# Kernel optimization log

Hardware: AMD Instinct MI355X
Metric: run time of the kernel (lower is better)

The kernel has to match this reference:

```python
import jax, jax.numpy as jnp
import numpy as np

B, C, H, W = 32, 3, 224, 224
P = 16                 # patch size
D = 768                # embed_size
NH = 12                # num heads
HD = D // NH           # head size
L = 12                 # depth
MLP = 4 * D
NC = 1000              # num classes
GH, GW = H // P, W // P
T = GH * GW            # tokens = 196
PATCH_DIM = P * P * C
EPS = 1e-5


def posemb_sincos_2d(h, w, dim, temperature=10000.0):
    yy, xx = jnp.meshgrid(jnp.arange(h, dtype=jnp.float32),
                          jnp.arange(w, dtype=jnp.float32), indexing='ij')
    omega = jnp.arange(dim // 4, dtype=jnp.float32) / (dim // 4 - 1)
    omega = 1.0 / (temperature ** omega)
    yv = yy.reshape(-1)[:, None] * omega[None, :]
    xv = xx.reshape(-1)[:, None] * omega[None, :]
    return jnp.concatenate([jnp.sin(xv), jnp.cos(xv), jnp.sin(yv), jnp.cos(yv)], axis=1)


def layernorm(x, g, b):
    mu = jnp.mean(x, axis=-1, keepdims=True)
    var = jnp.mean((x - mu) ** 2, axis=-1, keepdims=True)
    return (x - mu) * jax.lax.rsqrt(var + EPS) * g + b


def setup_inputs() -> dict:
    key = jax.random.key(0)
    ks = jax.random.split(key, 16)
    s = 0.02
    inp = {
        'x': jax.random.normal(ks[0], (B, C, H, W), jnp.float32),
        'embed_W': jax.random.normal(ks[1], (PATCH_DIM, D), jnp.float32) * s,
        'embed_b': jnp.zeros((D,), jnp.float32),
        'Wq': jax.random.normal(ks[2], (L, NH, D, HD), jnp.float32) * s,
        'Wk': jax.random.normal(ks[3], (L, NH, D, HD), jnp.float32) * s,
        'Wv': jax.random.normal(ks[4], (L, NH, D, HD), jnp.float32) * s,
        'Wo': jax.random.normal(ks[5], (L, D, D), jnp.float32) * s,
        'bo': jnp.zeros((L, D), jnp.float32),
        'ln1_g': jnp.ones((L, D), jnp.float32),
        'ln1_b': jnp.zeros((L, D), jnp.float32),
        'ln2_g': jnp.ones((L, D), jnp.float32),
        'ln2_b': jnp.zeros((L, D), jnp.float32),
        'W1': jax.random.normal(ks[6], (L, D, MLP), jnp.float32) * s,
        'b1': jnp.zeros((L, MLP), jnp.float32),
        'W2': jax.random.normal(ks[7], (L, MLP, D), jnp.float32) * s,
        'b2': jnp.zeros((L, D), jnp.float32),
        'head_W': jax.random.normal(ks[8], (D, NC), jnp.float32) * s,
    }
    return inp


def reference(x, embed_W, embed_b, Wq, Wk, Wv, Wo, bo,
              ln1_g, ln1_b, ln2_g, ln2_b, W1, b1, W2, b2, head_W):
    # patchify: b c (h p1) (w p2) -> b (h w) (p1 p2 c)
    p = x.reshape(B, C, GH, P, GW, P)
    p = p.transpose(0, 2, 4, 3, 5, 1).reshape(B, T, PATCH_DIM)
    h = p @ embed_W + embed_b + posemb_sincos_2d(GH, GW, D)[None]  # [B,T,D]

    scale = HD ** -0.5
    for l in range(L):
        xn = layernorm(h, ln1_g[l], ln1_b[l])
        q = jnp.einsum('btd,hde->bhte', xn, Wq[l])
        k = jnp.einsum('btd,hde->bhte', xn, Wk[l])
        v = jnp.einsum('btd,hde->bhte', xn, Wv[l])
        scores = jax.nn.softmax(jnp.einsum('bhte,bhse->bhts', q, k) * scale, axis=-1)
        att = jnp.einsum('bhts,bhse->bhte', scores, v)
        att = att.transpose(0, 2, 1, 3).reshape(B, T, D)  # concat heads
        h = h + att @ Wo[l] + bo[l]
        xn = layernorm(h, ln2_g[l], ln2_b[l])
        h = h + jax.nn.gelu(xn @ W1[l] + b1[l], approximate=False) @ W2[l] + b2[l]

    return h.mean(axis=1) @ head_W  # [B, NC]
```

## Files before the change

### kernel.cpp

```cpp
#include <hip/hip_runtime.h>
#include <cstdint>


typedef __bf16 bf16_t;
typedef __bf16 bf16x8 __attribute__((ext_vector_type(8)));
typedef __bf16 bf16x4 __attribute__((ext_vector_type(4)));
typedef float  f32x4  __attribute__((ext_vector_type(4)));

#define NLAYER 12
#define BMPAD 56
#define PSTRIDE 4816896l

__device__ __forceinline__ void g2lds16(const void* g, void* l) {
  __builtin_amdgcn_global_load_lds(
      (const __attribute__((address_space(1))) void*)g,
      (__attribute__((address_space(3))) void*)l, 16, 0, 0);
}

__global__ __launch_bounds__(256) void tcvt(
    const float* __restrict__ in, bf16_t* __restrict__ out,
    int R, int C, long inStride, long outOuter, long outInner, int innerN)
{
  int bi = blockIdx.z;
  in  += (long)bi * inStride;
  out += (long)(bi / innerN) * outOuter + (long)(bi % innerN) * outInner;
  __shared__ float t[32][33];
  int c0 = blockIdx.x * 32, r0 = blockIdx.y * 32;
  int tx = threadIdx.x, ty = threadIdx.y;
  #pragma unroll
  for (int i = ty; i < 32; i += 8) {
    int r = r0 + i, c = c0 + tx;
    if (r < R && c < C) t[i][tx] = in[(long)r * C + c];
  }
  __syncthreads();
  #pragma unroll
  for (int i = ty; i < 32; i += 8) {
    int c = c0 + i, r = r0 + tx;
    if (r < R && c < C) out[(long)c * R + r] = (bf16_t)t[tx][i];
  }
}

__global__ __launch_bounds__(256) void patchify(
    const float* __restrict__ x, bf16_t* __restrict__ patches)
{
  int idx = blockIdx.x * 256 + threadIdx.x;
  int bt = idx / 768, pd = idx % 768;
  int b = bt / 196, t = bt % 196;
  int gh = t / 14, gw = t % 14;
  int p1 = pd / 48, rem = pd % 48;
  int p2 = rem / 3, c = rem % 3;
  float v = x[(((long)(b * 3 + c) * 224) + gh * 16 + p1) * 224 + gw * 16 + p2];
  patches[idx] = (bf16_t)v;
}

__global__ __launch_bounds__(256) void hinit(
    const float* __restrict__ eb, float* __restrict__ h)
{
  int idx = blockIdx.x * 256 + threadIdx.x;
  int t = idx / 768, d = idx % 768;
  int gh = t / 14, gw = t % 14;
  int quadrant = d / 192, i = d % 192;
  float omega = powf(10000.0f, -(float)i / 191.0f);
  float arg = (quadrant < 2 ? (float)gw : (float)gh) * omega;
  float pv = ((quadrant & 1) == 0) ? sinf(arg) : cosf(arg);
  float v = pv + eb[d];
  #pragma unroll
  for (int b = 0; b < 32; ++b) h[(long)b * 150528 + idx] = v;
}

__global__ __launch_bounds__(256) void ln_fuse(
    float* __restrict__ h, const bf16_t* __restrict__ pbuf,
    const float* __restrict__ bias, const float* __restrict__ g,
    const float* __restrict__ bb, bf16_t* __restrict__ xn)
{
  int row = blockIdx.x * 4 + (threadIdx.x >> 6);
  int lane = threadIdx.x & 63;
  float* hr = h + (long)row * 768;
  const bf16_t* p0 = pbuf + (long)row * 768;
  const bf16_t* p1 = p0 + PSTRIDE;
  float4 v[3];
  float s = 0.f, s2 = 0.f;
  #pragma unroll
  for (int i = 0; i < 3; ++i) {
    int c4 = lane + 64 * i;
    float4 hv = ((const float4*)hr)[c4];
    bf16x4 q0 = *(const bf16x4*)(p0 + c4 * 4);
    bf16x4 q1 = *(const bf16x4*)(p1 + c4 * 4);
    float4 bv = {0.f, 0.f, 0.f, 0.f};
    if (bias) bv = ((const float4*)bias)[c4];
    hv.x += (float)q0[0] + (float)q1[0] + bv.x;
    hv.y += (float)q0[1] + (float)q1[1] + bv.y;
    hv.z += (float)q0[2] + (float)q1[2] + bv.z;
    hv.w += (float)q0[3] + (float)q1[3] + bv.w;
    ((float4*)hr)[c4] = hv;
    v[i] = hv;
    s  += hv.x + hv.y + hv.z + hv.w;
    s2 += hv.x * hv.x + hv.y * hv.y + hv.z * hv.z + hv.w * hv.w;
  }
  #pragma unroll
  for (int d = 1; d < 64; d <<= 1) {
    s  += __shfl_xor(s, d, 64);
    s2 += __shfl_xor(s2, d, 64);
  }
  float mu = s * (1.0f / 768.0f);
  float var = s2 * (1.0f / 768.0f) - mu * mu;
  float rs = rsqrtf(var + 1e-5f);
  uint2* outv = (uint2*)(xn + (long)row * 768);
  const float4* gv = (const float4*)g;
  const float4* bv2 = (const float4*)bb;
  #pragma unroll
  for (int i = 0; i < 3; ++i) {
    int c4 = lane + 64 * i;
    float4 gg = gv[c4], b4 = bv2[c4];
    union { bf16_t q[4]; uint2 u; } pk;
    pk.q[0] = (bf16_t)((v[i].x - mu) * rs * gg.x + b4.x);
    pk.q[1] = (bf16_t)((v[i].y - mu) * rs * gg.y + b4.y);
    pk.q[2] = (bf16_t)((v[i].z - mu) * rs * gg.z + b4.z);
    pk.q[3] = (bf16_t)((v[i].w - mu) * rs * gg.w + b4.w);
    outv[c4] = pk.u;
  }
}

template <int EPI>
__global__ __launch_bounds__(256) void gemm_bt(
    const bf16_t* __restrict__ A, const bf16_t* __restrict__ Bt,
    int Ktot, int KS, int ldc, int Mstore, int Nstore,
    const float* __restrict__ bias,
    float* __restrict__ fout, bf16_t* __restrict__ bout)
{
  int lin = blockIdx.x;
  int bm = lin % BMPAD;
  if (bm * 128 >= Mstore) return;
  int rest = lin / BMPAD;
  int ks = rest % KS;
  int bn = rest / KS;
  int Ksl = Ktot / KS;
  int k0 = ks * Ksl;

  __shared__ __align__(16) bf16_t As[128 * 32];
  __shared__ __align__(16) bf16_t Bs[128 * 32];
  int tid = threadIdx.x;
  int wave = tid >> 6, lane = tid & 63, quad = lane >> 4, l16 = lane & 15;
  int wm = wave >> 1, wn = wave & 1;
  const bf16_t* Ab = A + (long)bm * 128 * Ktot;
  const bf16_t* Bb = Bt + (long)bn * 128 * Ktot;

  f32x4 zero = {0.f, 0.f, 0.f, 0.f};
  f32x4 acc[4][4];
  #pragma unroll
  for (int i = 0; i < 4; ++i)
    #pragma unroll
    for (int j = 0; j < 4; ++j) acc[i][j] = zero;

  int f0 = tid * 16;
  int row0 = f0 >> 6;
  int ke0 = (f0 & 63) >> 1;

  for (int kt = k0; kt < k0 + Ksl; kt += 32) {
    __syncthreads();
    g2lds16(Ab + (long)row0 * Ktot + kt + ke0,        (char*)As + f0);
    g2lds16(Ab + (long)(row0 + 64) * Ktot + kt + ke0, (char*)As + f0 + 4096);
    g2lds16(Bb + (long)row0 * Ktot + kt + ke0,        (char*)Bs + f0);
    g2lds16(Bb + (long)(row0 + 64) * Ktot + kt + ke0, (char*)Bs + f0 + 4096);
    __syncthreads();

    bf16x8 af[4], bfr[4];
    #pragma unroll
    for (int i = 0; i < 4; ++i)
      af[i] = *(const bf16x8*)(As + (wm * 64 + i * 16 + l16) * 32 + quad * 8);
    #pragma unroll
    for (int j = 0; j < 4; ++j)
      bfr[j] = *(const bf16x8*)(Bs + (wn * 64 + j * 16 + l16) * 32 + quad * 8);
    #pragma unroll
    for (int i = 0; i < 4; ++i)
      #pragma unroll
      for (int j = 0; j < 4; ++j)
        acc[i][j] = __builtin_amdgcn_mfma_f32_16x16x32_bf16(af[i], bfr[j], acc[i][j], 0, 0, 0);
  }

  int m0 = bm * 128 + wm * 64, n0 = bn * 128 + wn * 64;
  #pragma unroll
  for (int i = 0; i < 4; ++i)
    #pragma unroll
    for (int j = 0; j < 4; ++j)
      #pragma unroll
      for (int r = 0; r < 4; ++r) {
        int row = m0 + i * 16 + quad * 4 + r;
        int col = n0 + j * 16 + l16;
        if (row >= Mstore || col >= Nstore) continue;
        float v = acc[i][j][r];
        if (EPI == 0) {
          bout[(long)row * ldc + col] = (bf16_t)v;
        } else if (EPI == 3) {
          float xg = v + bias[col];
          bout[(long)row * ldc + col] =
              (bf16_t)(0.5f * xg * (1.0f + erff(xg * 0.70710678118654752f)));
        } else if (EPI == 4) {
          fout[(long)row * ldc + col] = v;
        } else {
          bout[(long)ks * PSTRIDE + (long)row * ldc + col] = (bf16_t)v;
        }
      }
}

__global__ __launch_bounds__(256) void vtrans(
    const bf16_t* __restrict__ qkv, bf16_t* __restrict__ Vt)
{
  int bh = blockIdx.z, b = bh / 12, h = bh % 12;
  __shared__ bf16_t t[32][33];
  int e0 = blockIdx.x * 32, s0 = blockIdx.y * 32;
  int tx = threadIdx.x, ty = threadIdx.y;
  #pragma unroll
  for (int i = ty; i < 32; i += 8) {
    int s = s0 + i;
    bf16_t v = (bf16_t)0.0f;
    if (s < 196) v = qkv[(long)(b * 196 + s) * 2304 + 1536 + h * 64 + e0 + tx];
    t[i][tx] = v;
  }
  __syncthreads();
  #pragma unroll
  for (int i = ty; i < 32; i += 8) {
    int e = e0 + i, s = s0 + tx;
    if (s < 224) Vt[(long)bh * 64 * 224 + (long)e * 224 + s] = t[tx][i];
  }
}

__global__ __launch_bounds__(64) void attn_fused(
    const bf16_t* __restrict__ qkv, const bf16_t* __restrict__ Vt,
    bf16_t* __restrict__ att)
{
  __shared__ __align__(16) bf16_t Pl[16 * 232];
  int mt = blockIdx.x, bh = blockIdx.y;
  int b = bh / 12, h = bh % 12;
  int lane = threadIdx.x, quad = lane >> 4, l16 = lane & 15;

  #pragma unroll
  for (int i = 0; i < 4; ++i) {
    int idx = lane + 64 * i;
    Pl[(idx >> 4) * 232 + 208 + (idx & 15)] = (bf16_t)0.0f;
  }

  f32x4 zero = {0.f, 0.f, 0.f, 0.f};
  f32x4 acc[13];
  #pragma unroll
  for (int nt = 0; nt < 13; ++nt) acc[nt] = zero;

  long qoff = (long)(b * 196 + mt * 16 + l16) * 2304 + h * 64;
  #pragma unroll
  for (int kk = 0; kk < 2; ++kk) {
    bf16x8 a = *(const bf16x8*)(qkv + qoff + kk * 32 + quad * 8);
    #pragma unroll
    for (int nt = 0; nt < 13; ++nt) {
      long koff = (long)(b * 196 + nt * 16 + l16) * 2304 + 768 + h * 64 + kk * 32 + quad * 8;
      bf16x8 bb = *(const bf16x8*)(qkv + koff);
      acc[nt] = __builtin_amdgcn_mfma_f32_16x16x32_bf16(a, bb, acc[nt], 0, 0, 0);
    }
  }

  float p[13][4];
  #pragma unroll
  for (int nt = 0; nt < 13; ++nt)
    #pragma unroll
    for (int r = 0; r < 4; ++r) {
      float v = acc[nt][r] * 0.125f;
      if (nt == 12 && l16 >= 4) v = -1e30f;
      p[nt][r] = v;
    }

  #pragma unroll
  for (int r = 0; r < 4; ++r) {
    float mx = -1e30f;
    #pragma unroll
    for (int nt = 0; nt < 13; ++nt) mx = fmaxf(mx, p[nt][r]);
    #pragma unroll
    for (int d = 1; d < 16; d <<= 1) mx = fmaxf(mx, __shfl_xor(mx, d, 64));
    float sm = 0.f;
    #pragma unroll
    for (int nt = 0; nt < 13; ++nt) {
      float e = expf(p[nt][r] - mx);
      p[nt][r] = e;
      sm += e;
    }
    #pragma unroll
    for (int d = 1; d < 16; d <<= 1) sm += __shfl_xor(sm, d, 64);
    float inv = 1.0f / sm;
    #pragma unroll
    for (int nt = 0; nt < 13; ++nt) p[nt][r] *= inv;
  }

  #pragma unroll
  for (int nt = 0; nt < 13; ++nt)
    #pragma unroll
    for (int r = 0; r < 4; ++r)
      Pl[(quad * 4 + r) * 232 + nt * 16 + l16] = (bf16_t)p[nt][r];
  __syncthreads();

  f32x4 pv[4];
  #pragma unroll
  for (int nt = 0; nt < 4; ++nt) pv[nt] = zero;
  const bf16_t* Vb = Vt + (long)bh * 64 * 224;
  #pragma unroll
  for (int ks = 0; ks < 7; ++ks) {
    bf16x8 a = *(const bf16x8*)(Pl + l16 * 232 + ks * 32 + quad * 8);
    #pragma unroll
    for (int nt = 0; nt < 4; ++nt) {
      bf16x8 bb = *(const bf16x8*)(Vb + (long)(nt * 16 + l16) * 224 + ks * 32 + quad * 8);
      pv[nt] = __builtin_amdgcn_mfma_f32_16x16x32_bf16(a, bb, pv[nt], 0, 0, 0);
    }
  }

  #pragma unroll
  for (int nt = 0; nt < 4; ++nt)
    #pragma unroll
    for (int r = 0; r < 4; ++r) {
      int t = mt * 16 + quad * 4 + r;
      if (t < 196)
        att[(long)(b * 196 + t) * 768 + h * 64 + nt * 16 + l16] = (bf16_t)pv[nt][r];
    }
}

__global__ __launch_bounds__(256) void meanpool_fuse(
    const float* __restrict__ h, const bf16_t* __restrict__ pbuf,
    const float* __restrict__ bias, bf16_t* __restrict__ hm)
{
  int d = blockIdx.y * 256 + threadIdx.x;
  int b = blockIdx.x;
  float s = 0.f;
  for (int t = 0; t < 196; ++t) {
    long idx = (long)(b * 196 + t) * 768 + d;
    s += h[idx] + (float)pbuf[idx] + (float)pbuf[idx + PSTRIDE];
  }
  hm[b * 768 + d] = (bf16_t)(s * (1.0f / 196.0f) + bias[d]);
}

extern "C" void kernel_launch(void* const* d_in, const int* in_sizes, int n_in,
                              void* d_out, int out_size, void* d_ws, size_t ws_size,
                              hipStream_t stream)
{
  const float* x       = (const float*)d_in[0];
  const float* embed_W = (const float*)d_in[1];
  const float* embed_b = (const float*)d_in[2];
  const float* Wq      = (const float*)d_in[3];
  const float* Wk      = (const float*)d_in[4];
  const float* Wv      = (const float*)d_in[5];
  const float* Wo      = (const float*)d_in[6];
  const float* bo      = (const float*)d_in[7];
  const float* ln1_g   = (const float*)d_in[8];
  const float* ln1_b   = (const float*)d_in[9];
  const float* ln2_g   = (const float*)d_in[10];
  const float* ln2_b   = (const float*)d_in[11];
  const float* W1      = (const float*)d_in[12];
  const float* b1      = (const float*)d_in[13];
  const float* W2      = (const float*)d_in[14];
  const float* b2      = (const float*)d_in[15];
  const float* head_W  = (const float*)d_in[16];

  char* p = (char*)d_ws;
  auto carve = [&](size_t bytes) {
    char* r = p;
    p += (bytes + 255) & ~(size_t)255;
    return r;
  };
  bf16_t* embed_Wt = (bf16_t*)carve(589824ull * 2);
  bf16_t* qkvT     = (bf16_t*)carve(21233664ull * 2);
  bf16_t* WoT      = (bf16_t*)carve(7077888ull * 2);
  bf16_t* W1T      = (bf16_t*)carve(28311552ull * 2);
  bf16_t* W2T      = (bf16_t*)carve(28311552ull * 2);
  bf16_t* headWt   = (bf16_t*)carve(786432ull * 2);
  bf16_t* patches  = (bf16_t*)carve(4816896ull * 2);
  float*  h        = (float*)carve(4816896ull * 4);
  bf16_t* xn       = (bf16_t*)carve(4816896ull * 2);
  bf16_t* qkv      = (bf16_t*)carve(14487552ull * 2);
  bf16_t* Vt       = (bf16_t*)carve(5505024ull * 2);
  bf16_t* hmlp     = (bf16_t*)carve(19267584ull * 2);
  bf16_t* att      = (bf16_t*)carve(4816896ull * 2);
  bf16_t* pbuf     = (bf16_t*)carve(2ull * PSTRIDE * 2);
  bf16_t* hm       = (bf16_t*)carve(98304ull * 2);
  (void)ws_size; (void)n_in; (void)in_sizes; (void)out_size;

  dim3 tb32(32, 8);

  tcvt<<<dim3(24, 24, 1),   tb32, 0, stream>>>(embed_W, embed_Wt, 768, 768, 0, 0, 0, 1);
  tcvt<<<dim3(24, 24, 12),  tb32, 0, stream>>>(Wo, WoT, 768, 768, 589824, 589824, 0, 1);
  tcvt<<<dim3(2, 24, 144),  tb32, 0, stream>>>(Wq, qkvT,           768, 64, 49152, 1769472, 49152, 12);
  tcvt<<<dim3(2, 24, 144),  tb32, 0, stream>>>(Wk, qkvT + 589824,  768, 64, 49152, 1769472, 49152, 12);
  tcvt<<<dim3(2, 24, 144),  tb32, 0, stream>>>(Wv, qkvT + 1179648, 768, 64, 49152, 1769472, 49152, 12);
  tcvt<<<dim3(96, 24, 12),  tb32, 0, stream>>>(W1, W1T, 768, 3072, 2359296, 2359296, 0, 1);
  tcvt<<<dim3(24, 96, 12),  tb32, 0, stream>>>(W2, W2T, 3072, 768, 2359296, 2359296, 0, 1);
  tcvt<<<dim3(32, 24, 1),   tb32, 0, stream>>>(head_W, headWt, 768, 1000, 0, 0, 0, 1);

  patchify<<<18816, 256, 0, stream>>>(x, patches);
  hinit<<<588, 256, 0, stream>>>(embed_b, h);

  gemm_bt<5><<<BMPAD * 6 * 2, 256, 0, stream>>>(
      patches, embed_Wt, 768, 2, 768, 6272, 768, nullptr, nullptr, pbuf);

  for (int l = 0; l < NLAYER; ++l) {
    ln_fuse<<<1568, 256, 0, stream>>>(
        h, pbuf, l == 0 ? nullptr : b2 + (l - 1) * 768,
        ln1_g + l * 768, ln1_b + l * 768, xn);
    gemm_bt<0><<<BMPAD * 18, 256, 0, stream>>>(
        xn, qkvT + (long)l * 1769472, 768, 1, 2304, 6272, 2304,
        nullptr, nullptr, qkv);
    vtrans<<<dim3(2, 7, 384), tb32, 0, stream>>>(qkv, Vt);
    attn_fused<<<dim3(13, 384), 64, 0, stream>>>(qkv, Vt, att);
    gemm_bt<5><<<BMPAD * 6 * 2, 256, 0, stream>>>(
        att, WoT + (long)l * 589824, 768, 2, 768, 6272, 768,
        nullptr, nullptr, pbuf);
    ln_fuse<<<1568, 256, 0, stream>>>(
        h, pbuf, bo + l * 768, ln2_g + l * 768, ln2_b + l * 768, xn);
    gemm_bt<3><<<BMPAD * 24, 256, 0, stream>>>(
        xn, W1T + (long)l * 2359296, 768, 1, 3072, 6272, 3072,
        b1 + l * 3072, nullptr, hmlp);
    gemm_bt<5><<<BMPAD * 6 * 2, 256, 0, stream>>>(
        hmlp, W2T + (long)l * 2359296, 3072, 2, 768, 6272, 768,
        nullptr, nullptr, pbuf);
  }

  meanpool_fuse<<<dim3(32, 3), 256, 0, stream>>>(h, pbuf, b2 + 11 * 768, hm);
  gemm_bt<4><<<BMPAD * 8, 256, 0, stream>>>(
      hm, headWt, 768, 1, 1000, 32, 1000, nullptr, (float*)d_out, nullptr);
}
```

Before: 3.833 ms.

## Template GEMM K dims, split W2 GEMM 4-way, use fast GELU and exp

Makes the GEMM K size and split count compile-time template parameters and sets launch bounds to allow 4 blocks per CU. The W2 GEMM now uses a 4-way split-K, with ln_fuse and meanpool summing a variable number of partial buffers. The exact erf GELU is replaced by a tanh approximation built on __expf, and softmax switches to __expf. The aim is to cut address arithmetic, improve occupancy and parallelism on the long-K GEMM, and reduce transcendental cost, at the price of approximation error in GELU and more partial-buffer traffic.

```diff
diff --git a/kernel.cpp b/kernel.cpp
--- a/kernel.cpp
+++ b/kernel.cpp
@@ -69,29 +69,31 @@
 }
 
 __global__ __launch_bounds__(256) void ln_fuse(
-    float* __restrict__ h, const bf16_t* __restrict__ pbuf,
+    float* __restrict__ h, const bf16_t* __restrict__ pbuf, int nparts,
     const float* __restrict__ bias, const float* __restrict__ g,
     const float* __restrict__ bb, bf16_t* __restrict__ xn)
 {
   int row = blockIdx.x * 4 + (threadIdx.x >> 6);
   int lane = threadIdx.x & 63;
   float* hr = h + (long)row * 768;
-  const bf16_t* p0 = pbuf + (long)row * 768;
-  const bf16_t* p1 = p0 + PSTRIDE;
+  const bf16_t* pr = pbuf + (long)row * 768;
   float4 v[3];
   float s = 0.f, s2 = 0.f;
   #pragma unroll
   for (int i = 0; i < 3; ++i) {
     int c4 = lane + 64 * i;
     float4 hv = ((const float4*)hr)[c4];
-    bf16x4 q0 = *(const bf16x4*)(p0 + c4 * 4);
-    bf16x4 q1 = *(const bf16x4*)(p1 + c4 * 4);
-    float4 bv = {0.f, 0.f, 0.f, 0.f};
-    if (bias) bv = ((const float4*)bias)[c4];
-    hv.x += (float)q0[0] + (float)q1[0] + bv.x;
-    hv.y += (float)q0[1] + (float)q1[1] + bv.y;
-    hv.z += (float)q0[2] + (float)q1[2] + bv.z;
-    hv.w += (float)q0[3] + (float)q1[3] + bv.w;
+    float4 acc = {0.f, 0.f, 0.f, 0.f};
+    for (int pp = 0; pp < nparts; ++pp) {
+      bf16x4 q = *(const bf16x4*)(pr + (long)pp * PSTRIDE + c4 * 4);
+      acc.x += (float)q[0]; acc.y += (float)q[1];
+      acc.z += (float)q[2]; acc.w += (float)q[3];
+    }
+    if (bias) {
+      float4 bv = ((const float4*)bias)[c4];
+      acc.x += bv.x; acc.y += bv.y; acc.z += bv.z; acc.w += bv.w;
+    }
+    hv.x += acc.x; hv.y += acc.y; hv.z += acc.z; hv.w += acc.w;
     ((float4*)hr)[c4] = hv;
     v[i] = hv;
     s  += hv.x + hv.y + hv.z + hv.w;
@@ -121,10 +123,17 @@
   }
 }
 
-template <int EPI>
-__global__ __launch_bounds__(256) void gemm_bt(
+__device__ __forceinline__ float gelu_fast(float x) {
+  float y = 0.7978845608f * (x + 0.044715f * x * x * x);
+  float e = __expf(2.0f * y);
+  float t = 1.0f - 2.0f / (e + 1.0f);
+  return 0.5f * x * (1.0f + t);
+}
+
+template <int EPI, int KTOT, int KS>
+__global__ __launch_bounds__(256, 4) void gemm_bt(
     const bf16_t* __restrict__ A, const bf16_t* __restrict__ Bt,
-    int Ktot, int KS, int ldc, int Mstore, int Nstore,
+    int ldc, int Mstore, int Nstore,
     const float* __restrict__ bias,
     float* __restrict__ fout, bf16_t* __restrict__ bout)
 {
@@ -134,7 +143,7 @@
   int rest = lin / BMPAD;
   int ks = rest % KS;
   int bn = rest / KS;
-  int Ksl = Ktot / KS;
+  constexpr int Ksl = KTOT / KS;
   int k0 = ks * Ksl;
 
   __shared__ __align__(16) bf16_t As[128 * 32];
@@ -142,8 +151,8 @@
   int tid = threadIdx.x;
   int wave = tid >> 6, lane = tid & 63, quad = lane >> 4, l16 = lane & 15;
   int wm = wave >> 1, wn = wave & 1;
-  const bf16_t* Ab = A + (long)bm * 128 * Ktot;
-  const bf16_t* Bb = Bt + (long)bn * 128 * Ktot;
+  const bf16_t* Ab = A + (long)bm * 128 * KTOT;
+  const bf16_t* Bb = Bt + (long)bn * 128 * KTOT;
 
   f32x4 zero = {0.f, 0.f, 0.f, 0.f};
   f32x4 acc[4][4];
@@ -158,10 +167,10 @@
 
   for (int kt = k0; kt < k0 + Ksl; kt += 32) {
     __syncthreads();
-    g2lds16(Ab + (long)row0 * Ktot + kt + ke0,        (char*)As + f0);
-    g2lds16(Ab + (long)(row0 + 64) * Ktot + kt + ke0, (char*)As + f0 + 4096);
-    g2lds16(Bb + (long)row0 * Ktot + kt + ke0,        (char*)Bs + f0);
-    g2lds16(Bb + (long)(row0 + 64) * Ktot + kt + ke0, (char*)Bs + f0 + 4096);
+    g2lds16(Ab + (long)row0 * KTOT + kt + ke0,        (char*)As + f0);
+    g2lds16(Ab + (long)(row0 + 64) * KTOT + kt + ke0, (char*)As + f0 + 4096);
+    g2lds16(Bb + (long)row0 * KTOT + kt + ke0,        (char*)Bs + f0);
+    g2lds16(Bb + (long)(row0 + 64) * KTOT + kt + ke0, (char*)Bs + f0 + 4096);
     __syncthreads();
 
     bf16x8 af[4], bfr[4];
@@ -192,9 +201,7 @@
         if (EPI == 0) {
           bout[(long)row * ldc + col] = (bf16_t)v;
         } else if (EPI == 3) {
-          float xg = v + bias[col];
-          bout[(long)row * ldc + col] =
-              (bf16_t)(0.5f * xg * (1.0f + erff(xg * 0.70710678118654752f)));
+          bout[(long)row * ldc + col] = (bf16_t)gelu_fast(v + bias[col]);
         } else if (EPI == 4) {
           fout[(long)row * ldc + col] = v;
         } else {
@@ -277,7 +284,7 @@
     float sm = 0.f;
     #pragma unroll
     for (int nt = 0; nt < 13; ++nt) {
-      float e = expf(p[nt][r] - mx);
+      float e = __expf(p[nt][r] - mx);
       p[nt][r] = e;
       sm += e;
     }
@@ -328,7 +335,10 @@
   float s = 0.f;
   for (int t = 0; t < 196; ++t) {
     long idx = (long)(b * 196 + t) * 768 + d;
-    s += h[idx] + (float)pbuf[idx] + (float)pbuf[idx + PSTRIDE];
+    float v = h[idx];
+    #pragma unroll
+    for (int pp = 0; pp < 4; ++pp) v += (float)pbuf[idx + pp * PSTRIDE];
+    s += v;
   }
   hm[b * 768 + d] = (bf16_t)(s * (1.0f / 196.0f) + bias[d]);
 }
@@ -374,7 +384,7 @@
   bf16_t* Vt       = (bf16_t*)carve(5505024ull * 2);
   bf16_t* hmlp     = (bf16_t*)carve(19267584ull * 2);
   bf16_t* att      = (bf16_t*)carve(4816896ull * 2);
-  bf16_t* pbuf     = (bf16_t*)carve(2ull * PSTRIDE * 2);
+  bf16_t* pbuf     = (bf16_t*)carve(4ull * PSTRIDE * 2);
   bf16_t* hm       = (bf16_t*)carve(98304ull * 2);
   (void)ws_size; (void)n_in; (void)in_sizes; (void)out_size;
 
@@ -392,32 +402,32 @@
   patchify<<<18816, 256, 0, stream>>>(x, patches);
   hinit<<<588, 256, 0, stream>>>(embed_b, h);
 
-  gemm_bt<5><<<BMPAD * 6 * 2, 256, 0, stream>>>(
-      patches, embed_Wt, 768, 2, 768, 6272, 768, nullptr, nullptr, pbuf);
+  gemm_bt<5, 768, 2><<<BMPAD * 6 * 2, 256, 0, stream>>>(
+      patches, embed_Wt, 768, 6272, 768, nullptr, nullptr, pbuf);
 
   for (int l = 0; l < NLAYER; ++l) {
     ln_fuse<<<1568, 256, 0, stream>>>(
-        h, pbuf, l == 0 ? nullptr : b2 + (l - 1) * 768,
+        h, pbuf, l == 0 ? 2 : 4, l == 0 ? nullptr : b2 + (l - 1) * 768,
         ln1_g + l * 768, ln1_b + l * 768, xn);
-    gemm_bt<0><<<BMPAD * 18, 256, 0, stream>>>(
-        xn, qkvT + (long)l * 1769472, 768, 1, 2304, 6272, 2304,
+    gemm_bt<0, 768, 1><<<BMPAD * 18, 256, 0, stream>>>(
+        xn, qkvT + (long)l * 1769472, 2304, 6272, 2304,
         nullptr, nullptr, qkv);
     vtrans<<<dim3(2, 7, 384), tb32, 0, stream>>>(qkv, Vt);
     attn_fused<<<dim3(13, 384), 64, 0, stream>>>(qkv, Vt, att);
-    gemm_bt<5><<<BMPAD * 6 * 2, 256, 0, stream>>>(
-        att, WoT + (long)l * 589824, 768, 2, 768, 6272, 768,
+    gemm_bt<5, 768, 2><<<BMPAD * 6 * 2, 256, 0, stream>>>(
+        att, WoT + (long)l * 589824, 768, 6272, 768,
         nullptr, nullptr, pbuf);
     ln_fuse<<<1568, 256, 0, stream>>>(
-        h, pbuf, bo + l * 768, ln2_g + l * 768, ln2_b + l * 768, xn);
-    gemm_bt<3><<<BMPAD * 24, 256, 0, stream>>>(
-        xn, W1T + (long)l * 2359296, 768, 1, 3072, 6272, 3072,
+        h, pbuf, 2, bo + l * 768, ln2_g + l * 768, ln2_b + l * 768, xn);
+    gemm_bt<3, 768, 1><<<BMPAD * 24, 256, 0, stream>>>(
+        xn, W1T + (long)l * 2359296, 3072, 6272, 3072,
         b1 + l * 3072, nullptr, hmlp);
-    gemm_bt<5><<<BMPAD * 6 * 2, 256, 0, stream>>>(
-        hmlp, W2T + (long)l * 2359296, 3072, 2, 768, 6272, 768,
+    gemm_bt<5, 3072, 4><<<BMPAD * 6 * 4, 256, 0, stream>>>(
+        hmlp, W2T + (long)l * 2359296, 768, 6272, 768,
         nullptr, nullptr, pbuf);
   }
 
   meanpool_fuse<<<dim3(32, 3), 256, 0, stream>>>(h, pbuf, b2 + 11 * 768, hm);
-  gemm_bt<4><<<BMPAD * 8, 256, 0, stream>>>(
-      hm, headWt, 768, 1, 1000, 32, 1000, nullptr, (float*)d_out, nullptr);
-}
+  gemm_bt<4, 768, 1><<<BMPAD * 8, 256, 0, stream>>>(
+      hm, headWt, 1000, 32, 1000, nullptr, (float*)d_out, nullptr);
+}
```

Result: faster. 3.556 ms (-7.2%).
